# Optimization experiments

Measured on AMD Instinct MI355X. Metric: run time of the kernel, lower is better.

## Reference

```python
import jax, jax.numpy as jnp
import numpy as np

N_NODES = 100000
N_EDGES = 3200000
D_FEAT = 128
HIDDEN = 16
N_CLASSES = 8


def setup_inputs() -> dict:
    key = jax.random.key(0)
    k1, k2, k3, k4 = jax.random.split(key, 4)
    x = jax.random.normal(k1, (N_NODES, D_FEAT), dtype=jnp.float32)
    edge_index = jax.random.randint(k2, (2, N_EDGES), 0, N_NODES, dtype=jnp.int64)
    W1 = jax.random.normal(k3, (D_FEAT, HIDDEN), dtype=jnp.float32) * (1.0 / np.sqrt(D_FEAT))
    b1 = jnp.zeros((HIDDEN,), dtype=jnp.float32)
    W2 = jax.random.normal(k4, (HIDDEN, N_CLASSES), dtype=jnp.float32) * (1.0 / np.sqrt(HIDDEN))
    b2 = jnp.zeros((N_CLASSES,), dtype=jnp.float32)
    return {"x": x, "edge_index": edge_index, "W1": W1, "b1": b1, "W2": W2, "b2": b2}


def _gcn_conv(x, W, b, src, dst, deg_inv_sqrt, n_nodes):
    h = x @ W  # [N, F_out]
    norm = deg_inv_sqrt[src] * deg_inv_sqrt[dst]  # [E']
    msg = h[src] * norm[:, None]  # gather + scale
    out = jax.ops.segment_sum(msg, dst, num_segments=n_nodes)  # scatter-add
    return out + b


def _prep_edges(edge_index, n_nodes):
    # add self-loops (PyG GCNConv default) and compute symmetric norm degrees
    loop = jnp.arange(n_nodes, dtype=edge_index.dtype)
    src = jnp.concatenate([edge_index[0], loop])
    dst = jnp.concatenate([edge_index[1], loop])
    deg = jax.ops.segment_sum(jnp.ones_like(dst, dtype=jnp.float32), dst,
                              num_segments=n_nodes)
    deg_inv_sqrt = jnp.where(deg > 0, jax.lax.rsqrt(jnp.maximum(deg, 1.0)), 0.0)
    return src, dst, deg_inv_sqrt


def reference(x, edge_index, W1, b1, W2, b2):
    n_nodes = x.shape[0]
    src, dst, deg_inv_sqrt = _prep_edges(edge_index, n_nodes)
    h = jax.nn.relu(_gcn_conv(x, W1, b1, src, dst, deg_inv_sqrt, n_nodes))
    logits = _gcn_conv(h, W2, b2, src, dst, deg_inv_sqrt, n_nodes)
    return jax.nn.log_softmax(logits, axis=1)
```

## Files before the change

### kernel.cpp

```cpp
#include <hip/hip_runtime.h>

#define N_NODES 100000
#define N_EDGES 3200000
#define D_FEAT 128
#define HIDDEN 16
#define NCLS 8


__global__ void k_deg_init(unsigned* __restrict__ deg) {
    int i = blockIdx.x * blockDim.x + threadIdx.x;
    if (i < N_NODES) deg[i] = 1u;
}

__global__ void k_deg_count(const int* __restrict__ dst, unsigned* __restrict__ deg) {
    int i = blockIdx.x * blockDim.x + threadIdx.x;
    if (i < N_EDGES) atomicAdd(&deg[dst[i]], 1u);
}

__global__ void k_dis(const unsigned* __restrict__ deg, float* __restrict__ dis) {
    int i = blockIdx.x * blockDim.x + threadIdx.x;
    if (i < N_NODES) dis[i] = rsqrtf((float)deg[i]);
}

__global__ __launch_bounds__(256) void k_gemm1(const float* __restrict__ x,
                                               const float* __restrict__ W1,
                                               const float* __restrict__ dis,
                                               float* __restrict__ hd1,
                                               float* __restrict__ agg1) {
    __shared__ float sW[D_FEAT * HIDDEN];
    __shared__ float sx[64][132];
    int tid = threadIdx.x;
    for (int t = tid; t < D_FEAT * HIDDEN; t += 256) sW[t] = W1[t];

    int node0 = blockIdx.x * 64;
    #pragma unroll
    for (int it = 0; it < 8; ++it) {
        int lin = it * 256 + tid;
        int r   = lin >> 5;
        int c4  = lin & 31;
        int row = node0 + r;
        float4 v = make_float4(0.f, 0.f, 0.f, 0.f);
        if (row < N_NODES)
            v = *(const float4*)(x + (size_t)row * D_FEAT + c4 * 4);
        *(float4*)(&sx[r][c4 * 4]) = v;
    }
    __syncthreads();

    int lr   = tid >> 2;
    int node = node0 + lr;
    int f0   = (tid & 3) * 4;
    if (node >= N_NODES) return;

    float a0 = 0.f, a1 = 0.f, a2 = 0.f, a3 = 0.f;
    #pragma unroll
    for (int k = 0; k < D_FEAT; ++k) {
        float xv = sx[lr][k];
        a0 += xv * sW[k * HIDDEN + f0 + 0];
        a1 += xv * sW[k * HIDDEN + f0 + 1];
        a2 += xv * sW[k * HIDDEN + f0 + 2];
        a3 += xv * sW[k * HIDDEN + f0 + 3];
    }
    float s = dis[node];
    float4 o = make_float4(a0 * s, a1 * s, a2 * s, a3 * s);
    *(float4*)(hd1 + (size_t)node * HIDDEN + f0) = o;
    *(float4*)(agg1 + (size_t)node * HIDDEN + f0) = o;
}

__global__ void k_scatter16(const int* __restrict__ src, const int* __restrict__ dst,
                            const float* __restrict__ hd, float* __restrict__ agg) {
    long long g = (long long)blockIdx.x * blockDim.x + threadIdx.x;
    if (g >= (long long)N_EDGES * HIDDEN) return;
    int e = (int)(g >> 4);
    int j = (int)(g & 15);
    atomicAdd(&agg[(size_t)dst[e] * HIDDEN + j], hd[(size_t)src[e] * HIDDEN + j]);
}

__global__ void k_scatter8(const int* __restrict__ src, const int* __restrict__ dst,
                           const float* __restrict__ hd, float* __restrict__ agg) {
    long long g = (long long)blockIdx.x * blockDim.x + threadIdx.x;
    if (g >= (long long)N_EDGES * NCLS) return;
    int e = (int)(g >> 3);
    int j = (int)(g & 7);
    atomicAdd(&agg[(size_t)dst[e] * NCLS + j], hd[(size_t)src[e] * NCLS + j]);
}

__global__ __launch_bounds__(256) void k_layer2(const float* __restrict__ agg1,
                                                const float* __restrict__ dis,
                                                const float* __restrict__ b1,
                                                const float* __restrict__ W2,
                                                float* __restrict__ hd2,
                                                float* __restrict__ agg2) {
    __shared__ float sW[HIDDEN * NCLS];
    __shared__ float sb[HIDDEN];
    int tid = threadIdx.x;
    if (tid < HIDDEN * NCLS) sW[tid] = W2[tid];
    if (tid < HIDDEN)        sb[tid] = b1[tid];
    __syncthreads();

    int i = blockIdx.x * 256 + tid;
    if (i >= N_NODES) return;
    float s = dis[i];

    float h[HIDDEN];
    const float4* ap = (const float4*)(agg1 + (size_t)i * HIDDEN);
    #pragma unroll
    for (int q = 0; q < 4; ++q) {
        float4 a = ap[q];
        h[q * 4 + 0] = fmaxf(s * a.x + sb[q * 4 + 0], 0.f);
        h[q * 4 + 1] = fmaxf(s * a.y + sb[q * 4 + 1], 0.f);
        h[q * 4 + 2] = fmaxf(s * a.z + sb[q * 4 + 2], 0.f);
        h[q * 4 + 3] = fmaxf(s * a.w + sb[q * 4 + 3], 0.f);
    }
    float o[NCLS];
    #pragma unroll
    for (int k = 0; k < NCLS; ++k) o[k] = 0.f;
    #pragma unroll
    for (int j = 0; j < HIDDEN; ++j) {
        float hv = h[j];
        #pragma unroll
        for (int k = 0; k < NCLS; ++k) o[k] += hv * sW[j * NCLS + k];
    }
    float4 o0 = make_float4(o[0] * s, o[1] * s, o[2] * s, o[3] * s);
    float4 o1 = make_float4(o[4] * s, o[5] * s, o[6] * s, o[7] * s);
    float4* h2 = (float4*)(hd2  + (size_t)i * NCLS);
    float4* a2 = (float4*)(agg2 + (size_t)i * NCLS);
    h2[0] = o0; h2[1] = o1;
    a2[0] = o0; a2[1] = o1;
}

__global__ void k_final(const float* __restrict__ agg2, const float* __restrict__ dis,
                        const float* __restrict__ b2, float* __restrict__ out) {
    int i = blockIdx.x * blockDim.x + threadIdx.x;
    if (i >= N_NODES) return;
    float s = dis[i];
    float l[NCLS];
    const float4* ap = (const float4*)(agg2 + (size_t)i * NCLS);
    float4 a0 = ap[0], a1 = ap[1];
    l[0] = s * a0.x + b2[0]; l[1] = s * a0.y + b2[1];
    l[2] = s * a0.z + b2[2]; l[3] = s * a0.w + b2[3];
    l[4] = s * a1.x + b2[4]; l[5] = s * a1.y + b2[5];
    l[6] = s * a1.z + b2[6]; l[7] = s * a1.w + b2[7];
    float m = l[0];
    #pragma unroll
    for (int k = 1; k < NCLS; ++k) m = fmaxf(m, l[k]);
    float sum = 0.f;
    #pragma unroll
    for (int k = 0; k < NCLS; ++k) sum += __expf(l[k] - m);
    float lse = logf(sum) + m;
    float4 r0 = make_float4(l[0] - lse, l[1] - lse, l[2] - lse, l[3] - lse);
    float4 r1 = make_float4(l[4] - lse, l[5] - lse, l[6] - lse, l[7] - lse);
    float4* op = (float4*)(out + (size_t)i * NCLS);
    op[0] = r0; op[1] = r1;
}

extern "C" void kernel_launch(void* const* d_in, const int* in_sizes, int n_in,
                              void* d_out, int out_size, void* d_ws, size_t ws_size,
                              hipStream_t stream) {
    const float* x  = (const float*)d_in[0];
    const int*   ei = (const int*)d_in[1];
    const float* W1 = (const float*)d_in[2];
    const float* b1 = (const float*)d_in[3];
    const float* W2 = (const float*)d_in[4];
    const float* b2 = (const float*)d_in[5];
    float* out = (float*)d_out;

    const int* src = ei;
    const int* dst = ei + N_EDGES;

    float* ws = (float*)d_ws;
    const size_t N = N_NODES;
    unsigned* deg = (unsigned*)ws;
    float* dis  = ws + N;
    float* hd1  = ws + 2 * N;
    float* agg1 = ws + 18 * N;
    float* hd2  = ws + 34 * N;
    float* agg2 = ws + 42 * N;

    const int TB = 256;
    int nb_nodes = (N_NODES + TB - 1) / TB;
    int nb_edges = (N_EDGES + TB - 1) / TB;

    k_deg_init<<<nb_nodes, TB, 0, stream>>>(deg);
    k_deg_count<<<nb_edges, TB, 0, stream>>>(dst, deg);
    k_dis<<<nb_nodes, TB, 0, stream>>>(deg, dis);

    k_gemm1<<<(N_NODES + 63) / 64, TB, 0, stream>>>(x, W1, dis, hd1, agg1);

    long long w16 = (long long)N_EDGES * HIDDEN;
    k_scatter16<<<(int)((w16 + TB - 1) / TB), TB, 0, stream>>>(src, dst, hd1, agg1);

    k_layer2<<<nb_nodes, TB, 0, stream>>>(agg1, dis, b1, W2, hd2, agg2);

    long long w8 = (long long)N_EDGES * NCLS;
    k_scatter8<<<(int)((w8 + TB - 1) / TB), TB, 0, stream>>>(src, dst, hd2, agg2);

    k_final<<<nb_nodes, TB, 0, stream>>>(agg2, dis, b2, out);
}
```

Before: 572.4 us.

## Build CSR by destination and replace atomic scatters with per-node gathers

Builds a CSR adjacency grouped by destination using a three-stage prefix scan over the degrees and an atomic fill, then replaces the per-element atomicAdd scatter kernels with per-node gather loops. Each gather is fused with the following per-node stage (layer-2 matmul, and the final log-softmax). This removes about 80M float atomics and the separate agg buffers and elementwise kernels. In exchange it adds scan and CSR-fill kernels, and the neighbor order within the CSR is nondeterministic. Gather loop lengths also vary from node to node.

```diff
diff --git a/kernel.cpp b/kernel.cpp
--- a/kernel.cpp
+++ b/kernel.cpp
@@ -5,11 +5,12 @@
 #define D_FEAT 128
 #define HIDDEN 16
 #define NCLS 8
+#define NB_SCAN ((N_NODES + 255) / 256)
 
 
 __global__ void k_deg_init(unsigned* __restrict__ deg) {
     int i = blockIdx.x * blockDim.x + threadIdx.x;
-    if (i < N_NODES) deg[i] = 1u;
+    if (i < N_NODES) deg[i] = 0u;
 }
 
 __global__ void k_deg_count(const int* __restrict__ dst, unsigned* __restrict__ deg) {
@@ -19,14 +20,58 @@
 
 __global__ void k_dis(const unsigned* __restrict__ deg, float* __restrict__ dis) {
     int i = blockIdx.x * blockDim.x + threadIdx.x;
-    if (i < N_NODES) dis[i] = rsqrtf((float)deg[i]);
+    if (i < N_NODES) dis[i] = rsqrtf((float)(deg[i] + 1u));
+}
+
+__global__ void k_scan1(const unsigned* __restrict__ deg, unsigned* __restrict__ rp,
+                        unsigned* __restrict__ bsum) {
+    __shared__ unsigned s[256];
+    int tid = threadIdx.x;
+    int i = blockIdx.x * 256 + tid;
+    unsigned v = (i < N_NODES) ? deg[i] : 0u;
+    s[tid] = v; __syncthreads();
+    for (int off = 1; off < 256; off <<= 1) {
+        unsigned t = (tid >= off) ? s[tid - off] : 0u;
+        __syncthreads();
+        s[tid] += t;
+        __syncthreads();
+    }
+    if (i < N_NODES) rp[i] = s[tid] - v;
+    if (tid == 255) bsum[blockIdx.x] = s[255];
+}
+
+__global__ void k_scan2(unsigned* __restrict__ bsum) {
+    __shared__ unsigned s[512];
+    int tid = threadIdx.x;
+    unsigned v = (tid < NB_SCAN) ? bsum[tid] : 0u;
+    s[tid] = v; __syncthreads();
+    for (int off = 1; off < 512; off <<= 1) {
+        unsigned t = (tid >= off) ? s[tid - off] : 0u;
+        __syncthreads();
+        s[tid] += t;
+        __syncthreads();
+    }
+    bsum[tid] = s[tid] - v;
+}
+
+__global__ void k_scan3(unsigned* __restrict__ rp, const unsigned* __restrict__ bsum) {
+    int i = blockIdx.x * blockDim.x + threadIdx.x;
+    if (i < N_NODES) rp[i] += bsum[i >> 8];
+}
+
+__global__ void k_csr_fill(const int* __restrict__ src, const int* __restrict__ dst,
+                           unsigned* __restrict__ rp, unsigned* __restrict__ csr) {
+    int e = blockIdx.x * blockDim.x + threadIdx.x;
+    if (e < N_EDGES) {
+        unsigned p = atomicAdd(&rp[dst[e]], 1u);
+        csr[p] = (unsigned)src[e];
+    }
 }
 
 __global__ __launch_bounds__(256) void k_gemm1(const float* __restrict__ x,
                                                const float* __restrict__ W1,
                                                const float* __restrict__ dis,
-                                               float* __restrict__ hd1,
-                                               float* __restrict__ agg1) {
+                                               float* __restrict__ hd1) {
     __shared__ float sW[D_FEAT * HIDDEN];
     __shared__ float sx[64][132];
     int tid = threadIdx.x;
@@ -61,96 +106,70 @@
         a3 += xv * sW[k * HIDDEN + f0 + 3];
     }
     float s = dis[node];
-    float4 o = make_float4(a0 * s, a1 * s, a2 * s, a3 * s);
-    *(float4*)(hd1 + (size_t)node * HIDDEN + f0) = o;
-    *(float4*)(agg1 + (size_t)node * HIDDEN + f0) = o;
-}
-
-__global__ void k_scatter16(const int* __restrict__ src, const int* __restrict__ dst,
-                            const float* __restrict__ hd, float* __restrict__ agg) {
-    long long g = (long long)blockIdx.x * blockDim.x + threadIdx.x;
-    if (g >= (long long)N_EDGES * HIDDEN) return;
-    int e = (int)(g >> 4);
-    int j = (int)(g & 15);
-    atomicAdd(&agg[(size_t)dst[e] * HIDDEN + j], hd[(size_t)src[e] * HIDDEN + j]);
-}
-
-__global__ void k_scatter8(const int* __restrict__ src, const int* __restrict__ dst,
-                           const float* __restrict__ hd, float* __restrict__ agg) {
-    long long g = (long long)blockIdx.x * blockDim.x + threadIdx.x;
-    if (g >= (long long)N_EDGES * NCLS) return;
-    int e = (int)(g >> 3);
-    int j = (int)(g & 7);
-    atomicAdd(&agg[(size_t)dst[e] * NCLS + j], hd[(size_t)src[e] * NCLS + j]);
-}
-
-__global__ __launch_bounds__(256) void k_layer2(const float* __restrict__ agg1,
-                                                const float* __restrict__ dis,
-                                                const float* __restrict__ b1,
-                                                const float* __restrict__ W2,
-                                                float* __restrict__ hd2,
-                                                float* __restrict__ agg2) {
-    __shared__ float sW[HIDDEN * NCLS];
-    __shared__ float sb[HIDDEN];
-    int tid = threadIdx.x;
-    if (tid < HIDDEN * NCLS) sW[tid] = W2[tid];
-    if (tid < HIDDEN)        sb[tid] = b1[tid];
+    *(float4*)(hd1 + (size_t)node * HIDDEN + f0) = make_float4(a0 * s, a1 * s, a2 * s, a3 * s);
+}
+
+__global__ __launch_bounds__(256) void k_gather16_l2(
+        const unsigned* __restrict__ rp, const unsigned* __restrict__ csr,
+        const float* __restrict__ hd1, const float* __restrict__ dis,
+        const float* __restrict__ b1, const float* __restrict__ W2,
+        float* __restrict__ hd2) {
+    __shared__ float sh[16][17];
+    __shared__ float sW2[HIDDEN * NCLS];
+    __shared__ float sb1[HIDDEN];
+    int tid = threadIdx.x;
+    if (tid < HIDDEN * NCLS) sW2[tid] = W2[tid];
+    if (tid < HIDDEN)        sb1[tid] = b1[tid];
+
+    int n = tid >> 4;
+    int j = tid & 15;
+    int node = blockIdx.x * 16 + n;
+
+    unsigned start = (node == 0) ? 0u : rp[node - 1];
+    unsigned end   = rp[node];
+    float acc = hd1[(size_t)node * HIDDEN + j];
+    for (unsigned e = start; e < end; ++e) {
+        unsigned s = csr[e];
+        acc += hd1[(size_t)s * HIDDEN + j];
+    }
+    float dv = dis[node];
     __syncthreads();
-
-    int i = blockIdx.x * 256 + tid;
-    if (i >= N_NODES) return;
-    float s = dis[i];
-
-    float h[HIDDEN];
-    const float4* ap = (const float4*)(agg1 + (size_t)i * HIDDEN);
-    #pragma unroll
-    for (int q = 0; q < 4; ++q) {
-        float4 a = ap[q];
-        h[q * 4 + 0] = fmaxf(s * a.x + sb[q * 4 + 0], 0.f);
-        h[q * 4 + 1] = fmaxf(s * a.y + sb[q * 4 + 1], 0.f);
-        h[q * 4 + 2] = fmaxf(s * a.z + sb[q * 4 + 2], 0.f);
-        h[q * 4 + 3] = fmaxf(s * a.w + sb[q * 4 + 3], 0.f);
-    }
-    float o[NCLS];
-    #pragma unroll
-    for (int k = 0; k < NCLS; ++k) o[k] = 0.f;
-    #pragma unroll
-    for (int j = 0; j < HIDDEN; ++j) {
-        float hv = h[j];
+    float h = fmaxf(dv * acc + sb1[j], 0.f);
+    sh[n][j] = h;
+    __syncthreads();
+    if (j < NCLS) {
+        float o = 0.f;
         #pragma unroll
-        for (int k = 0; k < NCLS; ++k) o[k] += hv * sW[j * NCLS + k];
-    }
-    float4 o0 = make_float4(o[0] * s, o[1] * s, o[2] * s, o[3] * s);
-    float4 o1 = make_float4(o[4] * s, o[5] * s, o[6] * s, o[7] * s);
-    float4* h2 = (float4*)(hd2  + (size_t)i * NCLS);
-    float4* a2 = (float4*)(agg2 + (size_t)i * NCLS);
-    h2[0] = o0; h2[1] = o1;
-    a2[0] = o0; a2[1] = o1;
-}
-
-__global__ void k_final(const float* __restrict__ agg2, const float* __restrict__ dis,
-                        const float* __restrict__ b2, float* __restrict__ out) {
-    int i = blockIdx.x * blockDim.x + threadIdx.x;
-    if (i >= N_NODES) return;
-    float s = dis[i];
-    float l[NCLS];
-    const float4* ap = (const float4*)(agg2 + (size_t)i * NCLS);
-    float4 a0 = ap[0], a1 = ap[1];
-    l[0] = s * a0.x + b2[0]; l[1] = s * a0.y + b2[1];
-    l[2] = s * a0.z + b2[2]; l[3] = s * a0.w + b2[3];
-    l[4] = s * a1.x + b2[4]; l[5] = s * a1.y + b2[5];
-    l[6] = s * a1.z + b2[6]; l[7] = s * a1.w + b2[7];
-    float m = l[0];
-    #pragma unroll
-    for (int k = 1; k < NCLS; ++k) m = fmaxf(m, l[k]);
-    float sum = 0.f;
-    #pragma unroll
-    for (int k = 0; k < NCLS; ++k) sum += __expf(l[k] - m);
-    float lse = logf(sum) + m;
-    float4 r0 = make_float4(l[0] - lse, l[1] - lse, l[2] - lse, l[3] - lse);
-    float4 r1 = make_float4(l[4] - lse, l[5] - lse, l[6] - lse, l[7] - lse);
-    float4* op = (float4*)(out + (size_t)i * NCLS);
-    op[0] = r0; op[1] = r1;
+        for (int m = 0; m < HIDDEN; ++m) o += sh[n][m] * sW2[m * NCLS + j];
+        hd2[(size_t)node * NCLS + j] = dv * o;
+    }
+}
+
+__global__ __launch_bounds__(256) void k_gather8_final(
+        const unsigned* __restrict__ rp, const unsigned* __restrict__ csr,
+        const float* __restrict__ hd2, const float* __restrict__ dis,
+        const float* __restrict__ b2, float* __restrict__ out) {
+    int tid = threadIdx.x;
+    int node = blockIdx.x * 32 + (tid >> 3);
+    int j = tid & 7;
+
+    unsigned start = (node == 0) ? 0u : rp[node - 1];
+    unsigned end   = rp[node];
+    float acc = hd2[(size_t)node * NCLS + j];
+    for (unsigned e = start; e < end; ++e)
+        acc += hd2[(size_t)csr[e] * NCLS + j];
+
+    float l = dis[node] * acc + b2[j];
+    float m = l;
+    m = fmaxf(m, __shfl_xor(m, 1, 8));
+    m = fmaxf(m, __shfl_xor(m, 2, 8));
+    m = fmaxf(m, __shfl_xor(m, 4, 8));
+    float ex = __expf(l - m);
+    float ssum = ex;
+    ssum += __shfl_xor(ssum, 1, 8);
+    ssum += __shfl_xor(ssum, 2, 8);
+    ssum += __shfl_xor(ssum, 4, 8);
+    out[(size_t)node * NCLS + j] = l - (logf(ssum) + m);
 }
 
 extern "C" void kernel_launch(void* const* d_in, const int* in_sizes, int n_in,
@@ -167,14 +186,15 @@
     const int* src = ei;
     const int* dst = ei + N_EDGES;
 
-    float* ws = (float*)d_ws;
+    unsigned* ws = (unsigned*)d_ws;
     const size_t N = N_NODES;
-    unsigned* deg = (unsigned*)ws;
-    float* dis  = ws + N;
-    float* hd1  = ws + 2 * N;
-    float* agg1 = ws + 18 * N;
-    float* hd2  = ws + 34 * N;
-    float* agg2 = ws + 42 * N;
+    unsigned* deg  = ws;
+    float*    dis  = (float*)(ws + N);
+    unsigned* rp   = ws + 2 * N;
+    unsigned* bsum = ws + 3 * N;
+    unsigned* csr  = ws + 3 * N + 512;
+    float*    hd1  = (float*)(ws + 3 * N + 512 + N_EDGES);
+    float*    hd2  = hd1 + 16 * N;
 
     const int TB = 256;
     int nb_nodes = (N_NODES + TB - 1) / TB;
@@ -184,15 +204,13 @@
     k_deg_count<<<nb_edges, TB, 0, stream>>>(dst, deg);
     k_dis<<<nb_nodes, TB, 0, stream>>>(deg, dis);
 
-    k_gemm1<<<(N_NODES + 63) / 64, TB, 0, stream>>>(x, W1, dis, hd1, agg1);
-
-    long long w16 = (long long)N_EDGES * HIDDEN;
-    k_scatter16<<<(int)((w16 + TB - 1) / TB), TB, 0, stream>>>(src, dst, hd1, agg1);
-
-    k_layer2<<<nb_nodes, TB, 0, stream>>>(agg1, dis, b1, W2, hd2, agg2);
-
-    long long w8 = (long long)N_EDGES * NCLS;
-    k_scatter8<<<(int)((w8 + TB - 1) / TB), TB, 0, stream>>>(src, dst, hd2, agg2);
-
-    k_final<<<nb_nodes, TB, 0, stream>>>(agg2, dis, b2, out);
-}
+    k_scan1<<<NB_SCAN, 256, 0, stream>>>(deg, rp, bsum);
+    k_scan2<<<1, 512, 0, stream>>>(bsum);
+    k_scan3<<<nb_nodes, TB, 0, stream>>>(rp, bsum);
+    k_csr_fill<<<nb_edges, TB, 0, stream>>>(src, dst, rp, csr);
+
+    k_gemm1<<<(N_NODES + 63) / 64, TB, 0, stream>>>(x, W1, dis, hd1);
+
+    k_gather16_l2<<<N_NODES / 16, TB, 0, stream>>>(rp, csr, hd1, dis, b1, W2, hd2);
+    k_gather8_final<<<N_NODES / 32, TB, 0, stream>>>(rp, csr, hd2, dis, b2, out);
+}
```

Result: slower. 693.2 us (+21.1%).
